# Kernel tuning notes

Measured on AMD Instinct MI355X. Metric: run time of the kernel, lower is better.

The kernel has to match this reference:

```python
import jax, jax.numpy as jnp
import numpy as np

N, D = 4096, 1024

def setup_inputs() -> dict:
    key = jax.random.key(0)
    ks = jax.random.split(key, 7)
    s = 1.0 / np.sqrt(D)
    return {
        "x": jax.random.normal(ks[0], (N, D), dtype=jnp.float32),
        "Wq": jax.random.uniform(ks[1], (D, D), jnp.float32, -s, s),
        "bq": jax.random.uniform(ks[2], (D,), jnp.float32, -s, s),
        "Wk": jax.random.uniform(ks[3], (D, D), jnp.float32, -s, s),
        "bk": jax.random.uniform(ks[4], (D,), jnp.float32, -s, s),
        "Wv": jax.random.uniform(ks[5], (D, D), jnp.float32, -s, s),
        "bv": jax.random.uniform(ks[6], (D,), jnp.float32, -s, s),
    }

def reference(x, Wq, bq, Wk, bk, Wv, bv):
    # Linear layers: y = x @ W^T + b (torch convention, W is [out, in]; here square)
    Q = x @ Wq.T + bq  # [N, D]
    K = x @ Wk.T + bk  # [N, D]
    V = x @ Wv.T + bv  # [N, D]
    scores = (Q @ K.T) / jnp.sqrt(jnp.asarray(x.shape[-1], x.dtype))  # [N, N]
    attn = jax.nn.softmax(scores, axis=-1)
    return attn @ V  # [N, D]
```

## Files before the change

kernel.cpp:

```cpp
#include <hip/hip_runtime.h>


#define N_TOK 4096
#define DDIM  1024

typedef short s16x4 __attribute__((ext_vector_type(4)));
typedef short s16x8 __attribute__((ext_vector_type(8)));
typedef float f32x4 __attribute__((ext_vector_type(4)));

__device__ inline short f2b(float f) {
  unsigned int u = __float_as_uint(f);
  unsigned int r = (u + 0x7FFFu + ((u >> 16) & 1u)) >> 16;
  return (short)(unsigned short)r;
}

__device__ __forceinline__ void gld_lds16(const short* g, short* l) {
  __builtin_amdgcn_global_load_lds(
      (const __attribute__((address_space(1))) unsigned int*)g,
      (__attribute__((address_space(3))) unsigned int*)l, 16, 0, 0);
}

__device__ __forceinline__ void xcd_remap(int gx, int& bx, int& by) {
  const int L = by * gx + bx;
  const int g = L & 7, h = L >> 3;
  by = g * 4 + (h & 3);
  bx = h >> 2;
}
__device__ __forceinline__ void xcd_remap16(int gx, int& bx, int& by) {
  const int L = by * gx + bx;
  const int g = L & 7, h = L >> 3;
  by = g * 2 + (h & 1);
  bx = h >> 1;
}

template<int BM, int BN, int BK, int MODE>
constexpr int lds_shorts() {
  return (MODE == 3 && BN * 136 > BM * BK + BN * BK) ? BN * 136
                                                     : BM * BK + BN * BK;
}

template<int BM, int BN, int BK, int MODE>
__device__ __forceinline__ void gemm_core(
    const short* __restrict__ A, const short* __restrict__ B,
    void* __restrict__ C, float* __restrict__ aux, short* smem,
    int K, int ld, int ldc, float scale, int row0, int col0)
{
  constexpr int WM = BM / 2, WN = BN / 2, AI = WM / 16, AJ = WN / 16;
  constexpr int CPR = BK / 8;
  constexpr int MASK = CPR - 1;
  constexpr int CA = BM * CPR / 256;
  constexpr int CB = BN * CPR / 256;
  constexpr int NH = BK / 32;
  short* As = smem;
  short* Bs = smem + BM * BK;

  const int tid  = threadIdx.x;
  const int wave = tid >> 6, lane = tid & 63;
  const int wm = wave >> 1, wn = wave & 1;
  const int quad = lane >> 4, lr = lane & 15;

  f32x4 acc[AI][AJ];
  #pragma unroll
  for (int i = 0; i < AI; i++)
    #pragma unroll
    for (int j = 0; j < AJ; j++) acc[i][j] = {0.f, 0.f, 0.f, 0.f};

  for (int kk = 0; kk < K; kk += BK) {
    __syncthreads();
    #pragma unroll
    for (int c = 0; c < CA; c++) {
      const int id = c * 256 + wave * 64 + lane;
      const int r = id / CPR, slot = id & MASK;
      const int q = slot ^ (r & MASK);
      gld_lds16(A + (size_t)(row0 + r) * ld + kk + q * 8,
                &As[(c * 256 + wave * 64) * 8]);
    }
    #pragma unroll
    for (int c = 0; c < CB; c++) {
      const int id = c * 256 + wave * 64 + lane;
      const int r = id / CPR, slot = id & MASK;
      const int q = slot ^ (r & MASK);
      gld_lds16(B + (size_t)(col0 + r) * ld + kk + q * 8,
                &Bs[(c * 256 + wave * 64) * 8]);
    }
    __syncthreads();

    #pragma unroll
    for (int h = 0; h < NH; h++) {
      s16x8 af[AI], bf[AJ];
      #pragma unroll
      for (int i = 0; i < AI; i++) {
        const int row = wm * WM + i * 16 + lr;
        const int ch = (h * 4 + quad) ^ (row & MASK);
        af[i] = *reinterpret_cast<const s16x8*>(&As[(row * CPR + ch) * 8]);
      }
      #pragma unroll
      for (int j = 0; j < AJ; j++) {
        const int row = wn * WN + j * 16 + lr;
        const int ch = (h * 4 + quad) ^ (row & MASK);
        bf[j] = *reinterpret_cast<const s16x8*>(&Bs[(row * CPR + ch) * 8]);
      }
      #pragma unroll
      for (int i = 0; i < AI; i++)
        #pragma unroll
        for (int j = 0; j < AJ; j++)
          acc[i][j] = __builtin_amdgcn_mfma_f32_16x16x32_bf16(af[i], bf[j], acc[i][j], 0, 0, 0);
    }
  }

  if constexpr (MODE == 0) {
    float bb[AJ];
    #pragma unroll
    for (int j = 0; j < AJ; j++) bb[j] = aux[col0 + wn * WN + j * 16 + lr];
    #pragma unroll
    for (int i = 0; i < AI; i++) {
      const int r0 = row0 + wm * WM + i * 16 + quad * 4;
      #pragma unroll
      for (int j = 0; j < AJ; j++) {
        const int c = col0 + wn * WN + j * 16 + lr;
        #pragma unroll
        for (int r = 0; r < 4; r++)
          ((short*)C)[(size_t)(r0 + r) * ldc + c] = f2b(acc[i][j][r] * scale + bb[j]);
      }
    }
  } else if constexpr (MODE == 1) {
    #pragma unroll
    for (int i = 0; i < AI; i++) {
      const int r0 = row0 + wm * WM + i * 16 + quad * 4;
      float ex[AJ][4];
      #pragma unroll
      for (int j = 0; j < AJ; j++) {
        const int c = col0 + wn * WN + j * 16 + lr;
        #pragma unroll
        for (int r = 0; r < 4; r++) {
          ex[j][r] = __expf(acc[i][j][r] * scale);
          ((short*)C)[(size_t)(r0 + r) * ldc + c] = f2b(ex[j][r]);
        }
      }
      #pragma unroll
      for (int r = 0; r < 4; r++) {
        float s = 0.f;
        #pragma unroll
        for (int j = 0; j < AJ; j++) s += ex[j][r];
        s += __shfl_xor(s, 1, 64);
        s += __shfl_xor(s, 2, 64);
        s += __shfl_xor(s, 4, 64);
        s += __shfl_xor(s, 8, 64);
        if (lr == 0) atomicAdd(&aux[r0 + r], s);
      }
    }
  } else if constexpr (MODE == 2) {
    #pragma unroll
    for (int i = 0; i < AI; i++) {
      const int r0 = row0 + wm * WM + i * 16 + quad * 4;
      float linv[4];
      #pragma unroll
      for (int r = 0; r < 4; r++) linv[r] = 1.0f / aux[r0 + r];
      #pragma unroll
      for (int j = 0; j < AJ; j++) {
        const int c = col0 + wn * WN + j * 16 + lr;
        #pragma unroll
        for (int r = 0; r < 4; r++)
          ((float*)C)[(size_t)(r0 + r) * ldc + c] = acc[i][j][r] * linv[r];
      }
    }
  } else {
    float bb[AJ];
    #pragma unroll
    for (int j = 0; j < AJ; j++) bb[j] = aux[col0 + wn * WN + j * 16 + lr];
    __syncthreads();
    short* trans = smem;
    #pragma unroll
    for (int i = 0; i < AI; i++) {
      const int rl = wm * WM + i * 16 + quad * 4;
      #pragma unroll
      for (int j = 0; j < AJ; j++) {
        const int cl = wn * WN + j * 16 + lr;
        s16x4 v;
        #pragma unroll
        for (int r = 0; r < 4; r++) v[r] = f2b(acc[i][j][r] * scale + bb[j]);
        *reinterpret_cast<s16x4*>(&trans[cl * 136 + rl]) = v;
      }
    }
    __syncthreads();
    #pragma unroll
    for (int s = 0; s < BM * BN / 8 / 256; s++) {
      const int u = s * 256 + tid;
      const int cc = u >> (31 - __builtin_clz(BM / 8));
      const int seg = u & (BM / 8 - 1);
      s16x8 v = *reinterpret_cast<const s16x8*>(&trans[cc * 136 + seg * 8]);
      *reinterpret_cast<s16x8*>(
          &((short*)C)[(size_t)(col0 + cc) * ldc + row0 + seg * 8]) = v;
    }
  }
}

#define XU  (N_TOK * DDIM / 8)
#define WU  (DDIM * DDIM / 8)
#define NCVT ((XU + 3 * WU) / 256)
__global__ __launch_bounds__(256)
void cvt_all(const float* __restrict__ x,  const float* __restrict__ wq,
             const float* __restrict__ wk, const float* __restrict__ wv,
             short* __restrict__ xb, short* __restrict__ wqb,
             short* __restrict__ wkb, short* __restrict__ wvb,
             float* __restrict__ rowsum)
{
  if (blockIdx.x >= NCVT) {
    float4 z = {0.f, 0.f, 0.f, 0.f};
    float4* p = reinterpret_cast<float4*>(rowsum) + threadIdx.x * 4;
    p[0] = z; p[1] = z; p[2] = z; p[3] = z;
    return;
  }
  int gid = blockIdx.x * 256 + threadIdx.x;
  const float* src; short* dst; int off;
  if (gid < XU)               { src = x;  dst = xb;  off = gid; }
  else if (gid < XU + WU)     { src = wq; dst = wqb; off = gid - XU; }
  else if (gid < XU + 2 * WU) { src = wk; dst = wkb; off = gid - XU - WU; }
  else                        { src = wv; dst = wvb; off = gid - XU - 2 * WU; }
  const float4* g = reinterpret_cast<const float4*>(src) + (size_t)off * 2;
  float4 a = g[0], b = g[1];
  s16x8 o;
  o[0] = f2b(a.x); o[1] = f2b(a.y); o[2] = f2b(a.z); o[3] = f2b(a.w);
  o[4] = f2b(b.x); o[5] = f2b(b.y); o[6] = f2b(b.z); o[7] = f2b(b.w);
  reinterpret_cast<s16x8*>(dst)[off] = o;
}

__global__ __launch_bounds__(256)
void k_qkv(const short* __restrict__ xb,
           const short* __restrict__ Wqb, const short* __restrict__ Wkb,
           const short* __restrict__ Wvb,
           const float* __restrict__ bq, const float* __restrict__ bk,
           const float* __restrict__ bv,
           short* __restrict__ Qb, short* __restrict__ Kb, short* __restrict__ Vt)
{
  __shared__ short smem[lds_shorts<128, 128, 64, 3>()];
  int bx = blockIdx.x, by = blockIdx.y;
  xcd_remap(DDIM / 128, bx, by);
  if (blockIdx.z == 0) {
    gemm_core<128, 128, 64, 0>(xb, Wqb, Qb, (float*)bq, smem, DDIM, DDIM, DDIM,
                               1.0f, by * 128, bx * 128);
  } else if (blockIdx.z == 1) {
    gemm_core<128, 128, 64, 0>(xb, Wkb, Kb, (float*)bk, smem, DDIM, DDIM, DDIM,
                               1.0f, by * 128, bx * 128);
  } else {
    gemm_core<128, 128, 64, 3>(xb, Wvb, Vt, (float*)bv, smem, DDIM, DDIM, N_TOK,
                               1.0f, by * 128, bx * 128);
  }
}

__global__ __launch_bounds__(256, 2)
void k_score(const short* __restrict__ Qb, const short* __restrict__ Kb,
             short* __restrict__ SP, float* __restrict__ rowsum)
{
  __shared__ short smem[lds_shorts<256, 128, 64, 1>()];
  int bx = blockIdx.x, by = blockIdx.y;
  xcd_remap16(N_TOK / 128, bx, by);
  gemm_core<256, 128, 64, 1>(Qb, Kb, SP, rowsum, smem, DDIM, DDIM, N_TOK,
                             0.03125f, by * 256, bx * 128);
}

__global__ __launch_bounds__(256)
void k_pv(const short* __restrict__ SP, const short* __restrict__ Vt,
          float* __restrict__ out, const float* __restrict__ rowsum)
{
  __shared__ short smem[lds_shorts<128, 64, 128, 2>()];
  int bx = blockIdx.x, by = blockIdx.y;
  xcd_remap(DDIM / 64, bx, by);
  gemm_core<128, 64, 128, 2>(SP, Vt, out, (float*)rowsum, smem, N_TOK, N_TOK,
                             DDIM, 1.0f, by * 128, bx * 64);
}

extern "C" void kernel_launch(void* const* d_in, const int* in_sizes, int n_in,
                              void* d_out, int out_size, void* d_ws, size_t ws_size,
                              hipStream_t stream)
{
  const float* x  = (const float*)d_in[0];
  const float* Wq = (const float*)d_in[1];
  const float* bq = (const float*)d_in[2];
  const float* Wk = (const float*)d_in[3];
  const float* bk = (const float*)d_in[4];
  const float* Wv = (const float*)d_in[5];
  const float* bv = (const float*)d_in[6];
  float* out = (float*)d_out;

  char* ws = (char*)d_ws;
  const size_t MB = 1024 * 1024;
  short* Qb  = (short*)(ws + 0 * MB);
  short* Kb  = (short*)(ws + 8 * MB);
  short* Vt  = (short*)(ws + 24 * MB);
  short* SP  = (short*)(ws + 32 * MB);
  short* xb  = (short*)(ws + 32 * MB);
  short* Wqb = (short*)(ws + 40 * MB);
  short* Wkb = (short*)(ws + 42 * MB);
  short* Wvb = (short*)(ws + 44 * MB);
  float* rowsum = (float*)(ws + 64 * MB);

  dim3 b256(256);

  cvt_all<<<dim3(NCVT + 1), b256, 0, stream>>>(
      x, Wq, Wk, Wv, xb, Wqb, Wkb, Wvb, rowsum);

  k_qkv<<<dim3(DDIM / 128, N_TOK / 128, 3), b256, 0, stream>>>(
      xb, Wqb, Wkb, Wvb, bq, bk, bv, Qb, Kb, Vt);

  k_score<<<dim3(N_TOK / 128, N_TOK / 256), b256, 0, stream>>>(
      Qb, Kb, SP, rowsum);

  k_pv<<<dim3(DDIM / 64, N_TOK / 128), b256, 0, stream>>>(
      SP, Vt, out, rowsum);
}
```

Measured before the change: 213.1 us.

## Add ring-buffered 512-thread GEMM for score and PV with split-K atomics

Adds a new gemm_ring routine with a 4-slot LDS ring, direct global-to-LDS loads, explicit vmcnt waits and barriers, and setprio around the MFMA blocks. The score and PV kernels move to it with 512-thread blocks and larger tiles (256x256 and 256x128). PV is split-K in two halves that accumulate into the output with float atomics, so cvt_all now also zeroes the output. The aim is to overlap loads with MFMA work and raise per-block reuse, at the cost of atomic traffic on the output and more LDS per block.

```diff
diff --git a/kernel.cpp b/kernel.cpp
--- a/kernel.cpp
+++ b/kernel.cpp
@@ -7,6 +7,13 @@
 typedef short s16x4 __attribute__((ext_vector_type(4)));
 typedef short s16x8 __attribute__((ext_vector_type(8)));
 typedef float f32x4 __attribute__((ext_vector_type(4)));
+
+#define VMCNT0() asm volatile("s_waitcnt vmcnt(0)" ::: "memory")
+#define VMCNT3() asm volatile("s_waitcnt vmcnt(3)" ::: "memory")
+#define VMCNT4() asm volatile("s_waitcnt vmcnt(4)" ::: "memory")
+#define BARRIER() do { asm volatile("" ::: "memory"); \
+                       __builtin_amdgcn_s_barrier();  \
+                       asm volatile("" ::: "memory"); } while (0)
 
 __device__ inline short f2b(float f) {
   unsigned int u = __float_as_uint(f);
@@ -123,7 +130,135 @@
           ((short*)C)[(size_t)(r0 + r) * ldc + c] = f2b(acc[i][j][r] * scale + bb[j]);
       }
     }
-  } else if constexpr (MODE == 1) {
+  } else {
+    float bb[AJ];
+    #pragma unroll
+    for (int j = 0; j < AJ; j++) bb[j] = aux[col0 + wn * WN + j * 16 + lr];
+    __syncthreads();
+    short* trans = smem;
+    #pragma unroll
+    for (int i = 0; i < AI; i++) {
+      const int rl = wm * WM + i * 16 + quad * 4;
+      #pragma unroll
+      for (int j = 0; j < AJ; j++) {
+        const int cl = wn * WN + j * 16 + lr;
+        s16x4 v;
+        #pragma unroll
+        for (int r = 0; r < 4; r++) v[r] = f2b(acc[i][j][r] * scale + bb[j]);
+        *reinterpret_cast<s16x4*>(&trans[cl * 136 + rl]) = v;
+      }
+    }
+    __syncthreads();
+    #pragma unroll
+    for (int s = 0; s < BM * BN / 8 / 256; s++) {
+      const int u = s * 256 + tid;
+      const int cc = u >> (31 - __builtin_clz(BM / 8));
+      const int seg = u & (BM / 8 - 1);
+      s16x8 v = *reinterpret_cast<const s16x8*>(&trans[cc * 136 + seg * 8]);
+      *reinterpret_cast<s16x8*>(
+          &((short*)C)[(size_t)(cc + col0) * ldc + row0 + seg * 8]) = v;
+    }
+  }
+}
+
+template<int BM, int BN, int RING, int LPT, int MODE>
+__device__ __forceinline__ void gemm_ring(
+    const short* __restrict__ A, const short* __restrict__ B,
+    void* __restrict__ C, float* __restrict__ aux, short* smem,
+    int K, int ld, int ldc, float scale, int row0, int col0)
+{
+  constexpr int BK = 32;
+  constexpr int WM = BM / 2, WN = BN / 4;
+  constexpr int AI = WM / 16, AJ = WN / 16, AH = AI / 2;
+  constexpr int SLOT = (BM + BN) * BK;
+  constexpr int ACH = BM * (BK / 8);
+  static_assert((BM + BN) * (BK / 8) == LPT * 512, "LPT mismatch");
+  static_assert(ACH % 512 == 0, "A/B staging boundary must be wave-aligned");
+
+  const int tid  = threadIdx.x;
+  const int wave = tid >> 6, lane = tid & 63;
+  const int wm = wave >> 2, wn = wave & 3;
+  const int quad = lane >> 4, lr = lane & 15;
+  const int ph8 = ((quad ^ (lr & 3) ^ ((lr >> 2) & 3)) * 8);
+
+  f32x4 acc[AI][AJ];
+  #pragma unroll
+  for (int i = 0; i < AI; i++)
+    #pragma unroll
+    for (int j = 0; j < AJ; j++) acc[i][j] = {0.f, 0.f, 0.f, 0.f};
+
+  const int NT = K / BK;
+
+  auto stage = [&](int t, int s, int c) {
+    const int id = c * 512 + tid;
+    const int r = id >> 2;
+    const int q = (id & 3) ^ (r & 3) ^ ((r >> 2) & 3);
+    const short* src = (id < ACH)
+        ? A + (size_t)(row0 + r) * ld + t * BK + q * 8
+        : B + (size_t)(col0 + r - BM) * ld + t * BK + q * 8;
+    gld_lds16(src, &smem[s * SLOT + (c * 512 + wave * 64) * 8]);
+  };
+
+  #pragma unroll
+  for (int c = 0; c < LPT; c++) stage(0, 0, c);
+  #pragma unroll
+  for (int c = 0; c < LPT; c++) stage(1, 1, c);
+  if constexpr (LPT == 3) VMCNT3(); else VMCNT4();
+  BARRIER();
+
+  int slot = 0;
+  for (int t = 0; t < NT; t++) {
+    const short* sA = &smem[slot * SLOT];
+    const short* sB = sA + BM * BK;
+    const bool pf = (t + 2) < NT;
+    int s2 = slot + 2; if (s2 >= RING) s2 -= RING;
+
+    s16x8 bf[AJ], af[AH];
+    #pragma unroll
+    for (int j = 0; j < AJ; j++) {
+      const int row = wn * WN + j * 16 + lr;
+      bf[j] = *reinterpret_cast<const s16x8*>(&sB[row * BK + ph8]);
+    }
+    #pragma unroll
+    for (int i = 0; i < AH; i++) {
+      const int row = wm * WM + i * 16 + lr;
+      af[i] = *reinterpret_cast<const s16x8*>(&sA[row * BK + ph8]);
+    }
+    if (pf) { stage(t + 2, s2, 0); stage(t + 2, s2, 1); }
+    BARRIER();
+    __builtin_amdgcn_s_setprio(1);
+    #pragma unroll
+    for (int i = 0; i < AH; i++)
+      #pragma unroll
+      for (int j = 0; j < AJ; j++)
+        acc[i][j] = __builtin_amdgcn_mfma_f32_16x16x32_bf16(af[i], bf[j], acc[i][j], 0, 0, 0);
+    __builtin_amdgcn_s_setprio(0);
+    BARRIER();
+
+    #pragma unroll
+    for (int i = 0; i < AH; i++) {
+      const int row = wm * WM + (AH + i) * 16 + lr;
+      af[i] = *reinterpret_cast<const s16x8*>(&sA[row * BK + ph8]);
+    }
+    if (pf) {
+      stage(t + 2, s2, 2);
+      if constexpr (LPT == 4) stage(t + 2, s2, 3);
+    }
+    BARRIER();
+    __builtin_amdgcn_s_setprio(1);
+    #pragma unroll
+    for (int i = 0; i < AH; i++)
+      #pragma unroll
+      for (int j = 0; j < AJ; j++)
+        acc[AH + i][j] = __builtin_amdgcn_mfma_f32_16x16x32_bf16(af[i], bf[j], acc[AH + i][j], 0, 0, 0);
+    __builtin_amdgcn_s_setprio(0);
+    if (pf) { if constexpr (LPT == 3) VMCNT3(); else VMCNT4(); }
+    else    { VMCNT0(); }
+    BARRIER();
+    slot++; if (slot == RING) slot = 0;
+  }
+
+  if constexpr (MODE == 1) {
     #pragma unroll
     for (int i = 0; i < AI; i++) {
       const int r0 = row0 + wm * WM + i * 16 + quad * 4;
@@ -149,7 +284,7 @@
         if (lr == 0) atomicAdd(&aux[r0 + r], s);
       }
     }
-  } else if constexpr (MODE == 2) {
+  } else {
     #pragma unroll
     for (int i = 0; i < AI; i++) {
       const int r0 = row0 + wm * WM + i * 16 + quad * 4;
@@ -161,36 +296,9 @@
         const int c = col0 + wn * WN + j * 16 + lr;
         #pragma unroll
         for (int r = 0; r < 4; r++)
-          ((float*)C)[(size_t)(r0 + r) * ldc + c] = acc[i][j][r] * linv[r];
-      }
-    }
-  } else {
-    float bb[AJ];
-    #pragma unroll
-    for (int j = 0; j < AJ; j++) bb[j] = aux[col0 + wn * WN + j * 16 + lr];
-    __syncthreads();
-    short* trans = smem;
-    #pragma unroll
-    for (int i = 0; i < AI; i++) {
-      const int rl = wm * WM + i * 16 + quad * 4;
-      #pragma unroll
-      for (int j = 0; j < AJ; j++) {
-        const int cl = wn * WN + j * 16 + lr;
-        s16x4 v;
-        #pragma unroll
-        for (int r = 0; r < 4; r++) v[r] = f2b(acc[i][j][r] * scale + bb[j]);
-        *reinterpret_cast<s16x4*>(&trans[cl * 136 + rl]) = v;
-      }
-    }
-    __syncthreads();
-    #pragma unroll
-    for (int s = 0; s < BM * BN / 8 / 256; s++) {
-      const int u = s * 256 + tid;
-      const int cc = u >> (31 - __builtin_clz(BM / 8));
-      const int seg = u & (BM / 8 - 1);
-      s16x8 v = *reinterpret_cast<const s16x8*>(&trans[cc * 136 + seg * 8]);
-      *reinterpret_cast<s16x8*>(
-          &((short*)C)[(size_t)(col0 + cc) * ldc + row0 + seg * 8]) = v;
+          atomicAdd(&((float*)C)[(size_t)(r0 + r) * ldc + c],
+                    acc[i][j][r] * linv[r]);
+      }
     }
   }
 }
@@ -198,17 +306,25 @@
 #define XU  (N_TOK * DDIM / 8)
 #define WU  (DDIM * DDIM / 8)
 #define NCVT ((XU + 3 * WU) / 256)
+#define NZB  1024
 __global__ __launch_bounds__(256)
 void cvt_all(const float* __restrict__ x,  const float* __restrict__ wq,
              const float* __restrict__ wk, const float* __restrict__ wv,
              short* __restrict__ xb, short* __restrict__ wqb,
              short* __restrict__ wkb, short* __restrict__ wvb,
-             float* __restrict__ rowsum)
+             float* __restrict__ rowsum, float* __restrict__ outz)
 {
   if (blockIdx.x >= NCVT) {
+    const int zb = blockIdx.x - NCVT;
     float4 z = {0.f, 0.f, 0.f, 0.f};
-    float4* p = reinterpret_cast<float4*>(rowsum) + threadIdx.x * 4;
-    p[0] = z; p[1] = z; p[2] = z; p[3] = z;
+    if (zb < NZB) {
+      float4* p = reinterpret_cast<float4*>(outz) +
+                  (size_t)zb * 1024 + threadIdx.x * 4;
+      p[0] = z; p[1] = z; p[2] = z; p[3] = z;
+    } else {
+      float4* p = reinterpret_cast<float4*>(rowsum) + threadIdx.x * 4;
+      p[0] = z; p[1] = z; p[2] = z; p[3] = z;
+    }
     return;
   }
   int gid = blockIdx.x * 256 + threadIdx.x;
@@ -248,26 +364,27 @@
   }
 }
 
-__global__ __launch_bounds__(256, 2)
+__global__ __launch_bounds__(512, 2)
 void k_score(const short* __restrict__ Qb, const short* __restrict__ Kb,
              short* __restrict__ SP, float* __restrict__ rowsum)
 {
-  __shared__ short smem[lds_shorts<256, 128, 64, 1>()];
+  __shared__ short smem[4 * (256 + 256) * 32];
   int bx = blockIdx.x, by = blockIdx.y;
-  xcd_remap16(N_TOK / 128, bx, by);
-  gemm_core<256, 128, 64, 1>(Qb, Kb, SP, rowsum, smem, DDIM, DDIM, N_TOK,
-                             0.03125f, by * 256, bx * 128);
-}
-
-__global__ __launch_bounds__(256)
+  xcd_remap16(16, bx, by);
+  gemm_ring<256, 256, 4, 4, 1>(Qb, Kb, SP, rowsum, smem, DDIM, DDIM, N_TOK,
+                               0.03125f, by * 256, bx * 256);
+}
+
+__global__ __launch_bounds__(512, 2)
 void k_pv(const short* __restrict__ SP, const short* __restrict__ Vt,
           float* __restrict__ out, const float* __restrict__ rowsum)
 {
-  __shared__ short smem[lds_shorts<128, 64, 128, 2>()];
+  __shared__ short smem[4 * (256 + 128) * 32];
   int bx = blockIdx.x, by = blockIdx.y;
-  xcd_remap(DDIM / 64, bx, by);
-  gemm_core<128, 64, 128, 2>(SP, Vt, out, (float*)rowsum, smem, N_TOK, N_TOK,
-                             DDIM, 1.0f, by * 128, bx * 64);
+  xcd_remap16(8, bx, by);
+  const int k0 = blockIdx.z * (N_TOK / 2);
+  gemm_ring<256, 128, 4, 3, 4>(SP + k0, Vt + k0, out, (float*)rowsum, smem,
+                               N_TOK / 2, N_TOK, DDIM, 1.0f, by * 256, bx * 128);
 }
 
 extern "C" void kernel_launch(void* const* d_in, const int* in_sizes, int n_in,
@@ -295,17 +412,17 @@
   short* Wvb = (short*)(ws + 44 * MB);
   float* rowsum = (float*)(ws + 64 * MB);
 
-  dim3 b256(256);
-
-  cvt_all<<<dim3(NCVT + 1), b256, 0, stream>>>(
-      x, Wq, Wk, Wv, xb, Wqb, Wkb, Wvb, rowsum);
+  dim3 b256(256), b512(512);
+
+  cvt_all<<<dim3(NCVT + NZB + 1), b256, 0, stream>>>(
+      x, Wq, Wk, Wv, xb, Wqb, Wkb, Wvb, rowsum, out);
 
   k_qkv<<<dim3(DDIM / 128, N_TOK / 128, 3), b256, 0, stream>>>(
       xb, Wqb, Wkb, Wvb, bq, bk, bv, Qb, Kb, Vt);
 
-  k_score<<<dim3(N_TOK / 128, N_TOK / 256), b256, 0, stream>>>(
+  k_score<<<dim3(N_TOK / 256, N_TOK / 256), b512, 0, stream>>>(
       Qb, Kb, SP, rowsum);
 
-  k_pv<<<dim3(DDIM / 64, N_TOK / 128), b256, 0, stream>>>(
+  k_pv<<<dim3(DDIM / 128, N_TOK / 256, 2), b512, 0, stream>>>(
       SP, Vt, out, rowsum);
 }
```

Measured after the change: 245.1 us. +15.0%, slower.

## Split PV GEMM along K into two halves with atomic accumulation into output

Applied to the files above, without the earlier changes.

The P·V GEMM now splits the 4096-long reduction into two halves along a z grid dimension and uses a 128x128 tile with BK 64. Each half adds its normalized partial result into the output with float atomics. The conversion kernel gets extra blocks that zero the output beforehand. The aim is more parallelism and a better tile shape for the PV stage, at the cost of atomic traffic and an extra output-zeroing pass.

```diff
diff --git a/kernel.cpp b/kernel.cpp
--- a/kernel.cpp
+++ b/kernel.cpp
@@ -164,6 +164,22 @@
           ((float*)C)[(size_t)(r0 + r) * ldc + c] = acc[i][j][r] * linv[r];
       }
     }
+  } else if constexpr (MODE == 4) {
+    #pragma unroll
+    for (int i = 0; i < AI; i++) {
+      const int r0 = row0 + wm * WM + i * 16 + quad * 4;
+      float linv[4];
+      #pragma unroll
+      for (int r = 0; r < 4; r++) linv[r] = 1.0f / aux[r0 + r];
+      #pragma unroll
+      for (int j = 0; j < AJ; j++) {
+        const int c = col0 + wn * WN + j * 16 + lr;
+        #pragma unroll
+        for (int r = 0; r < 4; r++)
+          atomicAdd(&((float*)C)[(size_t)(r0 + r) * ldc + c],
+                    acc[i][j][r] * linv[r]);
+      }
+    }
   } else {
     float bb[AJ];
     #pragma unroll
@@ -198,17 +214,25 @@
 #define XU  (N_TOK * DDIM / 8)
 #define WU  (DDIM * DDIM / 8)
 #define NCVT ((XU + 3 * WU) / 256)
+#define NZB  1024
 __global__ __launch_bounds__(256)
 void cvt_all(const float* __restrict__ x,  const float* __restrict__ wq,
              const float* __restrict__ wk, const float* __restrict__ wv,
              short* __restrict__ xb, short* __restrict__ wqb,
              short* __restrict__ wkb, short* __restrict__ wvb,
-             float* __restrict__ rowsum)
+             float* __restrict__ rowsum, float* __restrict__ outz)
 {
   if (blockIdx.x >= NCVT) {
+    const int zb = blockIdx.x - NCVT;
     float4 z = {0.f, 0.f, 0.f, 0.f};
-    float4* p = reinterpret_cast<float4*>(rowsum) + threadIdx.x * 4;
-    p[0] = z; p[1] = z; p[2] = z; p[3] = z;
+    if (zb < NZB) {
+      float4* p = reinterpret_cast<float4*>(outz) +
+                  (size_t)zb * 1024 + threadIdx.x * 4;
+      p[0] = z; p[1] = z; p[2] = z; p[3] = z;
+    } else {
+      float4* p = reinterpret_cast<float4*>(rowsum) + threadIdx.x * 4;
+      p[0] = z; p[1] = z; p[2] = z; p[3] = z;
+    }
     return;
   }
   int gid = blockIdx.x * 256 + threadIdx.x;
@@ -263,11 +287,12 @@
 void k_pv(const short* __restrict__ SP, const short* __restrict__ Vt,
           float* __restrict__ out, const float* __restrict__ rowsum)
 {
-  __shared__ short smem[lds_shorts<128, 64, 128, 2>()];
+  __shared__ short smem[lds_shorts<128, 128, 64, 4>()];
   int bx = blockIdx.x, by = blockIdx.y;
-  xcd_remap(DDIM / 64, bx, by);
-  gemm_core<128, 64, 128, 2>(SP, Vt, out, (float*)rowsum, smem, N_TOK, N_TOK,
-                             DDIM, 1.0f, by * 128, bx * 64);
+  xcd_remap(DDIM / 128, bx, by);
+  const int k0 = blockIdx.z * (N_TOK / 2);
+  gemm_core<128, 128, 64, 4>(SP + k0, Vt + k0, out, (float*)rowsum, smem,
+                             N_TOK / 2, N_TOK, DDIM, 1.0f, by * 128, bx * 128);
 }
 
 extern "C" void kernel_launch(void* const* d_in, const int* in_sizes, int n_in,
@@ -297,8 +322,8 @@
 
   dim3 b256(256);
 
-  cvt_all<<<dim3(NCVT + 1), b256, 0, stream>>>(
-      x, Wq, Wk, Wv, xb, Wqb, Wkb, Wvb, rowsum);
+  cvt_all<<<dim3(NCVT + NZB + 1), b256, 0, stream>>>(
+      x, Wq, Wk, Wv, xb, Wqb, Wkb, Wvb, rowsum, out);
 
   k_qkv<<<dim3(DDIM / 128, N_TOK / 128, 3), b256, 0, stream>>>(
       xb, Wqb, Wkb, Wvb, bq, bk, bv, Qb, Kb, Vt);
@@ -306,6 +331,6 @@
   k_score<<<dim3(N_TOK / 128, N_TOK / 256), b256, 0, stream>>>(
       Qb, Kb, SP, rowsum);
 
-  k_pv<<<dim3(DDIM / 64, N_TOK / 128), b256, 0, stream>>>(
+  k_pv<<<dim3(DDIM / 128, N_TOK / 128, 2), b256, 0, stream>>>(
       SP, Vt, out, rowsum);
 }
```

Measured after the change: 229.7 us. 1.08x slower.

## Rewrite score kernel with double-buffered direct-to-LDS loads and swizzled tiles

Applied to the files above, without the earlier changes.

Replaces the generic 256x128 score GEMM with a dedicated 128x128 kernel that double-buffers Q/K tiles in LDS using global_load_lds, an XOR swizzle to avoid bank conflicts, and explicit vmcnt/lgkmcnt waits. Prefetch of tile t+2 is issued right after the fragments are read, and MFMA issue priority is raised, so loads overlap with compute. The grid changes to 32x32 blocks and uses a different XCD remap. The exp/rowsum epilogue is moved inline. The hand-written waitcnt and barrier scheduling adds fragility, and the smaller tile lowers data reuse per block.

```diff
diff --git a/kernel.cpp b/kernel.cpp
--- a/kernel.cpp
+++ b/kernel.cpp
@@ -7,6 +7,13 @@
 typedef short s16x4 __attribute__((ext_vector_type(4)));
 typedef short s16x8 __attribute__((ext_vector_type(8)));
 typedef float f32x4 __attribute__((ext_vector_type(4)));
+
+#define VMCNT0() asm volatile("s_waitcnt vmcnt(0)" ::: "memory")
+#define VMCNT8() asm volatile("s_waitcnt vmcnt(8)" ::: "memory")
+#define LGKMCNT0() asm volatile("s_waitcnt lgkmcnt(0)" ::: "memory")
+#define BARRIER() do { asm volatile("" ::: "memory"); \
+                       __builtin_amdgcn_s_barrier();  \
+                       asm volatile("" ::: "memory"); } while (0)
 
 __device__ inline short f2b(float f) {
   unsigned int u = __float_as_uint(f);
@@ -123,32 +130,6 @@
           ((short*)C)[(size_t)(r0 + r) * ldc + c] = f2b(acc[i][j][r] * scale + bb[j]);
       }
     }
-  } else if constexpr (MODE == 1) {
-    #pragma unroll
-    for (int i = 0; i < AI; i++) {
-      const int r0 = row0 + wm * WM + i * 16 + quad * 4;
-      float ex[AJ][4];
-      #pragma unroll
-      for (int j = 0; j < AJ; j++) {
-        const int c = col0 + wn * WN + j * 16 + lr;
-        #pragma unroll
-        for (int r = 0; r < 4; r++) {
-          ex[j][r] = __expf(acc[i][j][r] * scale);
-          ((short*)C)[(size_t)(r0 + r) * ldc + c] = f2b(ex[j][r]);
-        }
-      }
-      #pragma unroll
-      for (int r = 0; r < 4; r++) {
-        float s = 0.f;
-        #pragma unroll
-        for (int j = 0; j < AJ; j++) s += ex[j][r];
-        s += __shfl_xor(s, 1, 64);
-        s += __shfl_xor(s, 2, 64);
-        s += __shfl_xor(s, 4, 64);
-        s += __shfl_xor(s, 8, 64);
-        if (lr == 0) atomicAdd(&aux[r0 + r], s);
-      }
-    }
   } else if constexpr (MODE == 2) {
     #pragma unroll
     for (int i = 0; i < AI; i++) {
@@ -190,7 +171,7 @@
       const int seg = u & (BM / 8 - 1);
       s16x8 v = *reinterpret_cast<const s16x8*>(&trans[cc * 136 + seg * 8]);
       *reinterpret_cast<s16x8*>(
-          &((short*)C)[(size_t)(col0 + cc) * ldc + row0 + seg * 8]) = v;
+          &((short*)C)[(size_t)(cc + col0) * ldc + row0 + seg * 8]) = v;
     }
   }
 }
@@ -252,11 +233,112 @@
 void k_score(const short* __restrict__ Qb, const short* __restrict__ Kb,
              short* __restrict__ SP, float* __restrict__ rowsum)
 {
-  __shared__ short smem[lds_shorts<256, 128, 64, 1>()];
+  constexpr int BM = 128, BN = 128, BK = 64;
+  constexpr int NT = DDIM / BK;
+  __shared__ short smem[2][(BM + BN) * BK];
+
   int bx = blockIdx.x, by = blockIdx.y;
-  xcd_remap16(N_TOK / 128, bx, by);
-  gemm_core<256, 128, 64, 1>(Qb, Kb, SP, rowsum, smem, DDIM, DDIM, N_TOK,
-                             0.03125f, by * 256, bx * 128);
+  xcd_remap(32, bx, by);
+  const int row0 = by * BM, col0 = bx * BN;
+
+  const int tid  = threadIdx.x;
+  const int wave = tid >> 6, lane = tid & 63;
+  const int wm = wave >> 1, wn = wave & 1;
+  const int quad = lane >> 4, lr = lane & 15;
+
+  auto stage = [&](int t, int sl) {
+    #pragma unroll
+    for (int c = 0; c < 8; c++) {
+      const int id = c * 256 + tid;
+      const int r  = id >> 3;
+      const int q  = (id & 7) ^ (r & 7);
+      const short* src = (r < BM)
+          ? Qb + (size_t)(row0 + r) * DDIM + t * BK + q * 8
+          : Kb + (size_t)(col0 + r - BM) * DDIM + t * BK + q * 8;
+      gld_lds16(src, &smem[sl][(c * 256 + wave * 64) * 8]);
+    }
+  };
+
+  f32x4 acc[4][4];
+  #pragma unroll
+  for (int i = 0; i < 4; i++)
+    #pragma unroll
+    for (int j = 0; j < 4; j++) acc[i][j] = {0.f, 0.f, 0.f, 0.f};
+
+  stage(0, 0);
+  stage(1, 1);
+  VMCNT8();
+  BARRIER();
+
+  for (int t = 0; t < NT; t++) {
+    const int sl = t & 1;
+    const short* As = smem[sl];
+    const short* Bs = smem[sl] + BM * BK;
+
+    s16x8 af[2][4], bf[2][4];
+    #pragma unroll
+    for (int h = 0; h < 2; h++) {
+      #pragma unroll
+      for (int i = 0; i < 4; i++) {
+        const int row = wm * 64 + i * 16 + lr;
+        const int ch = (h * 4 + quad) ^ (row & 7);
+        af[h][i] = *reinterpret_cast<const s16x8*>(&As[(row * 8 + ch) * 8]);
+      }
+      #pragma unroll
+      for (int j = 0; j < 4; j++) {
+        const int row = wn * 64 + j * 16 + lr;
+        const int ch = (h * 4 + quad) ^ (row & 7);
+        bf[h][j] = *reinterpret_cast<const s16x8*>(&Bs[(row * 8 + ch) * 8]);
+      }
+    }
+    LGKMCNT0();
+    __builtin_amdgcn_sched_barrier(0);
+    BARRIER();
+
+    const bool pf = (t + 2) < NT;
+    if (pf) stage(t + 2, sl);
+
+    __builtin_amdgcn_s_setprio(1);
+    #pragma unroll
+    for (int h = 0; h < 2; h++)
+      #pragma unroll
+      for (int i = 0; i < 4; i++)
+        #pragma unroll
+        for (int j = 0; j < 4; j++)
+          acc[i][j] = __builtin_amdgcn_mfma_f32_16x16x32_bf16(
+              af[h][i], bf[h][j], acc[i][j], 0, 0, 0);
+    __builtin_amdgcn_s_setprio(0);
+
+    if (pf) { VMCNT8(); } else { VMCNT0(); }
+    BARRIER();
+  }
+
+  constexpr float scale = 0.03125f;
+  #pragma unroll
+  for (int i = 0; i < 4; i++) {
+    const int r0 = row0 + wm * 64 + i * 16 + quad * 4;
+    float ex[4][4];
+    #pragma unroll
+    for (int j = 0; j < 4; j++) {
+      const int c = col0 + wn * 64 + j * 16 + lr;
+      #pragma unroll
+      for (int r = 0; r < 4; r++) {
+        ex[j][r] = __expf(acc[i][j][r] * scale);
+        SP[(size_t)(r0 + r) * N_TOK + c] = f2b(ex[j][r]);
+      }
+    }
+    #pragma unroll
+    for (int r = 0; r < 4; r++) {
+      float s = 0.f;
+      #pragma unroll
+      for (int j = 0; j < 4; j++) s += ex[j][r];
+      s += __shfl_xor(s, 1, 64);
+      s += __shfl_xor(s, 2, 64);
+      s += __shfl_xor(s, 4, 64);
+      s += __shfl_xor(s, 8, 64);
+      if (lr == 0) atomicAdd(&rowsum[r0 + r], s);
+    }
+  }
 }
 
 __global__ __launch_bounds__(256)
@@ -303,8 +385,7 @@
   k_qkv<<<dim3(DDIM / 128, N_TOK / 128, 3), b256, 0, stream>>>(
       xb, Wqb, Wkb, Wvb, bq, bk, bv, Qb, Kb, Vt);
 
-  k_score<<<dim3(N_TOK / 128, N_TOK / 256), b256, 0, stream>>>(
-      Qb, Kb, SP, rowsum);
+  k_score<<<dim3(32, 32), b256, 0, stream>>>(Qb, Kb, SP, rowsum);
 
   k_pv<<<dim3(DDIM / 64, N_TOK / 128), b256, 0, stream>>>(
       SP, Vt, out, rowsum);
```

Result: faster. 207.1 us (-2.8%).
